# Kernel tuning notes

Hardware: AMD Instinct MI355X
Metric: run time of the kernel (lower is better)

Reference implementation:

```python
import jax, jax.numpy as jnp
import numpy as np
from jax import lax

H = 64  # hidden_size

def _lstm_layer(x, w_ih, w_hh, b_ih, b_hh):
    # x: (B, T, in). PyTorch gate order [i, f, g, o]; gates = x@W_ih^T + h@W_hh^T + b_ih + b_hh.
    B, T, _ = x.shape
    xw = jnp.einsum('bti,gi->btg', x, w_ih) + (b_ih + b_hh)  # (B, T, 4H), input projection hoisted out of scan

    def step(carry, xw_t):
        h, c = carry
        gates = xw_t + h @ w_hh.T                     # (B, 4H)
        i, f, g, o = jnp.split(gates, 4, axis=-1)
        i = jax.nn.sigmoid(i)
        f = jax.nn.sigmoid(f)
        g = jnp.tanh(g)
        o = jax.nn.sigmoid(o)
        c = f * c + i * g
        h = o * jnp.tanh(c)
        return (h, c), h

    h0 = jnp.zeros((B, H), dtype=x.dtype)
    c0 = jnp.zeros((B, H), dtype=x.dtype)
    (h_n, _), hs = lax.scan(step, (h0, c0), jnp.swapaxes(xw, 0, 1))  # hs: (T, B, H)
    return jnp.swapaxes(hs, 0, 1), h_n


def setup_inputs() -> dict:
    key = jax.random.key(0)
    ks = jax.random.split(key, 12)
    s = 1.0 / np.sqrt(H)  # PyTorch LSTM init scale
    return {
        'x':     jax.random.normal(ks[0], (2048, 512, 4), dtype=jnp.float32),
        'w_ih0': jax.random.uniform(ks[1], (4 * H, 4), jnp.float32, -s, s),
        'w_hh0': jax.random.uniform(ks[2], (4 * H, H), jnp.float32, -s, s),
        'b_ih0': jax.random.uniform(ks[3], (4 * H,), jnp.float32, -s, s),
        'b_hh0': jax.random.uniform(ks[4], (4 * H,), jnp.float32, -s, s),
        'w_ih1': jax.random.uniform(ks[5], (4 * H, H), jnp.float32, -s, s),
        'w_hh1': jax.random.uniform(ks[6], (4 * H, H), jnp.float32, -s, s),
        'b_ih1': jax.random.uniform(ks[7], (4 * H,), jnp.float32, -s, s),
        'b_hh1': jax.random.uniform(ks[8], (4 * H,), jnp.float32, -s, s),
        'fc_w':  jax.random.uniform(ks[9], (H, H), jnp.float32, -s, s),
        'fc_b':  jax.random.uniform(ks[10], (H,), jnp.float32, -s, s),
    }


def reference(x, w_ih0, w_hh0, b_ih0, b_hh0, w_ih1, w_hh1, b_ih1, b_hh1, fc_w, fc_b):
    # 2-layer LSTM (eval mode: inter-layer dropout inactive), take last layer's final hidden,
    # then Linear + tanh.
    h1_seq, _ = _lstm_layer(x, w_ih0, w_hh0, b_ih0, b_hh0)
    _, h_n = _lstm_layer(h1_seq, w_ih1, w_hh1, b_ih1, b_hh1)
    return jnp.tanh(h_n @ fc_w.T + fc_b)
```

## Files before the change

kernel.cpp:

```cpp
#include <hip/hip_runtime.h>


#define HID 64
#define TSTEPS 512
#define MB 8
#define BLK 512
#define HSTR 72
#define LOG2E  1.4426950408889634f
#define LOG2E2 2.8853900817779268f

typedef _Float16 f16;
typedef _Float16 half8 __attribute__((ext_vector_type(8)));
typedef _Float16 half4 __attribute__((ext_vector_type(4)));
typedef float f32x4 __attribute__((ext_vector_type(4)));

__device__ __forceinline__ float sig2(float y) {
    return __builtin_amdgcn_rcpf(1.0f + __builtin_amdgcn_exp2f(-y));
}
__device__ __forceinline__ float tanh2(float y) {
    return fmaf(2.0f, __builtin_amdgcn_rcpf(1.0f + __builtin_amdgcn_exp2f(-y)), -1.0f);
}

__global__ __launch_bounds__(BLK, 2) void lstm_mfma(
    const float* __restrict__ x,
    const float* __restrict__ w_ih0,
    const float* __restrict__ w_hh0,
    const float* __restrict__ b_ih0,
    const float* __restrict__ b_hh0,
    const float* __restrict__ w_ih1,
    const float* __restrict__ w_hh1,
    const float* __restrict__ b_ih1,
    const float* __restrict__ b_hh1,
    const float* __restrict__ fc_w,
    const float* __restrict__ fc_b,
    float* __restrict__ out)
{
    __shared__ f16 xs[TSTEPS * MB * 4];
    __shared__ f16 h0s[2][MB * HSTR];
    __shared__ f16 h1s[2][MB * HSTR];

    const int tid  = threadIdx.x;
    const int w    = tid >> 6;
    const int l    = tid & 63;
    const int quad = l >> 4;
    const int l15  = l & 15;
    const int wl   = w & 3;
    const bool isL0 = (w < 4);
    const int b0   = blockIdx.x * MB;

    for (int it = tid; it < MB * TSTEPS; it += BLK) {
        const int m = it >> 9;
        const int t = it & 511;
        const float4 v = *((const float4*)x + (size_t)(b0 + m) * TSTEPS + t);
        *(half4*)(xs + (t * MB + m) * 4) =
            (half4){ (f16)v.x, (f16)v.y, (f16)v.z, (f16)v.w };
    }
    for (int it = tid; it < MB * HSTR; it += BLK) {
        h0s[0][it] = (f16)0.f; h0s[1][it] = (f16)0.f;
        h1s[0][it] = (f16)0.f; h1s[1][it] = (f16)0.f;
    }

    half8 Bf[4][4];
    float biasr[4];
    const half8 Z = { (f16)0.f,(f16)0.f,(f16)0.f,(f16)0.f,
                      (f16)0.f,(f16)0.f,(f16)0.f,(f16)0.f };
    #pragma unroll
    for (int ti = 0; ti < 4; ++ti) {
        const int n = (wl + 4 * ti) * 16 + l15;
        const float sc = (ti == 2) ? LOG2E2 : LOG2E;
        if (isL0) {
            biasr[ti] = (b_ih0[n] + b_hh0[n]) * sc;
            half8 pz = Z;
            if (quad == 0) {
                const float4 v = *(const float4*)(w_ih0 + n * 4);
                pz[0] = (f16)(v.x * sc); pz[1] = (f16)(v.y * sc);
                pz[2] = (f16)(v.z * sc); pz[3] = (f16)(v.w * sc);
            }
            Bf[ti][0] = pz;
            #pragma unroll
            for (int ks = 0; ks < 2; ++ks) {
                const int ko = ks * 32 + quad * 8;
                const float4 a = *(const float4*)(w_hh0 + n * HID + ko);
                const float4 b = *(const float4*)(w_hh0 + n * HID + ko + 4);
                Bf[ti][1 + ks] = (half8){
                    (f16)(a.x*sc),(f16)(a.y*sc),(f16)(a.z*sc),(f16)(a.w*sc),
                    (f16)(b.x*sc),(f16)(b.y*sc),(f16)(b.z*sc),(f16)(b.w*sc) };
            }
            Bf[ti][3] = Z;
        } else {
            biasr[ti] = (b_ih1[n] + b_hh1[n]) * sc;
            #pragma unroll
            for (int ks = 0; ks < 2; ++ks) {
                const int ko = ks * 32 + quad * 8;
                const float4 a = *(const float4*)(w_ih1 + n * HID + ko);
                const float4 b = *(const float4*)(w_ih1 + n * HID + ko + 4);
                Bf[ti][ks] = (half8){
                    (f16)(a.x*sc),(f16)(a.y*sc),(f16)(a.z*sc),(f16)(a.w*sc),
                    (f16)(b.x*sc),(f16)(b.y*sc),(f16)(b.z*sc),(f16)(b.w*sc) };
                const float4 c = *(const float4*)(w_hh1 + n * HID + ko);
                const float4 d = *(const float4*)(w_hh1 + n * HID + ko + 4);
                Bf[ti][2 + ks] = (half8){
                    (f16)(c.x*sc),(f16)(c.y*sc),(f16)(c.z*sc),(f16)(c.w*sc),
                    (f16)(d.x*sc),(f16)(d.y*sc),(f16)(d.z*sc),(f16)(d.w*sc) };
            }
        }
    }

    const bool lo   = (quad < 2);
    const int  mrow = (quad & 1) * 4 + (lo ? 0 : 2);
    const int  uu   = wl * 16 + l15;
    const int  hb   = (l15 & 7) * HSTR + quad * 8;
    float cst0 = 0.f, cst1 = 0.f;
    __syncthreads();

    #pragma unroll 1
    for (int r = 0; r <= TSTEPS; ++r) {
        const int pr = r & 1;
        const int pv = pr ^ 1;

        if (isL0) {
            if (r < TSTEPS) {
                const half4 xv = *(const half4*)(xs + (r * MB + (l15 & 7)) * 4);
                half8 ax = Z;
                if (quad == 0) { ax[0]=xv[0]; ax[1]=xv[1]; ax[2]=xv[2]; ax[3]=xv[3]; }
                const half8 A1 = *(const half8*)(h0s[pv] + hb);
                const half8 A2 = *(const half8*)(h0s[pv] + hb + 32);
                f32x4 g[4];
                #pragma unroll
                for (int ti = 0; ti < 4; ++ti) {
                    f32x4 acc = { biasr[ti], biasr[ti], biasr[ti], biasr[ti] };
                    acc   = __builtin_amdgcn_mfma_f32_16x16x32_f16(ax, Bf[ti][0], acc, 0, 0, 0);
                    acc   = __builtin_amdgcn_mfma_f32_16x16x32_f16(A1, Bf[ti][1], acc, 0, 0, 0);
                    g[ti] = __builtin_amdgcn_mfma_f32_16x16x32_f16(A2, Bf[ti][2], acc, 0, 0, 0);
                }
                #pragma unroll
                for (int j = 0; j < 2; ++j) {
                    const float pi = lo ? g[0][j] : g[0][2 + j];
                    const float pf = lo ? g[1][j] : g[1][2 + j];
                    const float pg = lo ? g[2][j] : g[2][2 + j];
                    const float po = lo ? g[3][j] : g[3][2 + j];
                    float& c = j ? cst1 : cst0;
                    c = sig2(pf) * c + sig2(pi) * tanh2(pg);
                    h0s[pr][(mrow + j) * HSTR + uu] =
                        (f16)(sig2(po) * tanh2(c * LOG2E2));
                }
            }
        } else {
            const half8 A1 = *(const half8*)(h0s[pv] + hb);
            const half8 A2 = *(const half8*)(h0s[pv] + hb + 32);
            const half8 A3 = *(const half8*)(h1s[pr] + hb);
            const half8 A4 = *(const half8*)(h1s[pr] + hb + 32);
            f32x4 g[4];
            #pragma unroll
            for (int ti = 0; ti < 4; ++ti) {
                f32x4 acc = { biasr[ti], biasr[ti], biasr[ti], biasr[ti] };
                acc   = __builtin_amdgcn_mfma_f32_16x16x32_f16(A1, Bf[ti][0], acc, 0, 0, 0);
                acc   = __builtin_amdgcn_mfma_f32_16x16x32_f16(A2, Bf[ti][1], acc, 0, 0, 0);
                acc   = __builtin_amdgcn_mfma_f32_16x16x32_f16(A3, Bf[ti][2], acc, 0, 0, 0);
                g[ti] = __builtin_amdgcn_mfma_f32_16x16x32_f16(A4, Bf[ti][3], acc, 0, 0, 0);
            }
            const float keep = (r > 0) ? 1.f : 0.f;
            #pragma unroll
            for (int j = 0; j < 2; ++j) {
                const float pi = lo ? g[0][j] : g[0][2 + j];
                const float pf = lo ? g[1][j] : g[1][2 + j];
                const float pg = lo ? g[2][j] : g[2][2 + j];
                const float po = lo ? g[3][j] : g[3][2 + j];
                float& c = j ? cst1 : cst0;
                c = keep * (sig2(pf) * c + sig2(pi) * tanh2(pg));
                h1s[pv][(mrow + j) * HSTR + uu] =
                    (f16)(keep * sig2(po) * tanh2(c * LOG2E2));
            }
        }
        __syncthreads();
    }

    {
        const int v = tid & 63;
        const int m = tid >> 6;
        float a = fc_b[v];
        const f16* hp = h1s[1] + m * HSTR;
        const float4* wp = (const float4*)(fc_w + v * HID);
        #pragma unroll
        for (int kk = 0; kk < HID / 4; ++kk) {
            const float4 wv = wp[kk];
            a += (float)hp[kk * 4 + 0] * wv.x + (float)hp[kk * 4 + 1] * wv.y
               + (float)hp[kk * 4 + 2] * wv.z + (float)hp[kk * 4 + 3] * wv.w;
        }
        out[(size_t)(b0 + m) * HID + v] = tanh2(a * LOG2E2);
    }
}

extern "C" void kernel_launch(void* const* d_in, const int* in_sizes, int n_in,
                              void* d_out, int out_size, void* d_ws, size_t ws_size,
                              hipStream_t stream) {
    const float* x     = (const float*)d_in[0];
    const float* w_ih0 = (const float*)d_in[1];
    const float* w_hh0 = (const float*)d_in[2];
    const float* b_ih0 = (const float*)d_in[3];
    const float* b_hh0 = (const float*)d_in[4];
    const float* w_ih1 = (const float*)d_in[5];
    const float* w_hh1 = (const float*)d_in[6];
    const float* b_ih1 = (const float*)d_in[7];
    const float* b_hh1 = (const float*)d_in[8];
    const float* fc_w  = (const float*)d_in[9];
    const float* fc_b  = (const float*)d_in[10];
    float* out = (float*)d_out;

    const int B = in_sizes[0] / (TSTEPS * 4);
    lstm_mfma<<<dim3(B / MB), dim3(BLK), 0, stream>>>(
        x, w_ih0, w_hh0, b_ih0, b_hh0, w_ih1, w_hh1, b_ih1, b_hh1, fc_w, fc_b, out);
}
```

Baseline: 381.7 us.

## Split LSTM step into alternating MFMA and activation phases across layers

Restructures the time loop so that each step is split into an MFMA phase and an activation/store phase. Layer-0 warps do their MFMAs while layer-1 warps run activations, and the reverse in the next phase. This is meant to balance matrix-core and VALU/transcendental work across the two warp groups. The layer-1 hidden state becomes single-buffered. The cost is twice as many block barriers per timestep, plus a manually unrolled prologue and epilogue.

```diff
diff --git a/kernel.cpp b/kernel.cpp
--- a/kernel.cpp
+++ b/kernel.cpp
@@ -37,7 +37,7 @@
 {
     __shared__ f16 xs[TSTEPS * MB * 4];
     __shared__ f16 h0s[2][MB * HSTR];
-    __shared__ f16 h1s[2][MB * HSTR];
+    __shared__ f16 h1s[MB * HSTR];
 
     const int tid  = threadIdx.x;
     const int w    = tid >> 6;
@@ -56,8 +56,7 @@
             (half4){ (f16)v.x, (f16)v.y, (f16)v.z, (f16)v.w };
     }
     for (int it = tid; it < MB * HSTR; it += BLK) {
-        h0s[0][it] = (f16)0.f; h0s[1][it] = (f16)0.f;
-        h1s[0][it] = (f16)0.f; h1s[1][it] = (f16)0.f;
+        h0s[0][it] = (f16)0.f; h0s[1][it] = (f16)0.f; h1s[it] = (f16)0.f;
     }
 
     half8 Bf[4][4];
@@ -111,75 +110,89 @@
     const int  uu   = wl * 16 + l15;
     const int  hb   = (l15 & 7) * HSTR + quad * 8;
     float cst0 = 0.f, cst1 = 0.f;
+    f32x4 g[4];
+
+    auto l0_mfma = [&](int r, const f16* h0rd) {
+        const half4 xv = *(const half4*)(xs + (r * MB + (l15 & 7)) * 4);
+        half8 ax = Z;
+        if (quad == 0) { ax[0]=xv[0]; ax[1]=xv[1]; ax[2]=xv[2]; ax[3]=xv[3]; }
+        const half8 A1 = *(const half8*)(h0rd + hb);
+        const half8 A2 = *(const half8*)(h0rd + hb + 32);
+        #pragma unroll
+        for (int ti = 0; ti < 4; ++ti) {
+            f32x4 acc = { biasr[ti], biasr[ti], biasr[ti], biasr[ti] };
+            acc   = __builtin_amdgcn_mfma_f32_16x16x32_f16(ax, Bf[ti][0], acc, 0, 0, 0);
+            acc   = __builtin_amdgcn_mfma_f32_16x16x32_f16(A1, Bf[ti][1], acc, 0, 0, 0);
+            g[ti] = __builtin_amdgcn_mfma_f32_16x16x32_f16(A2, Bf[ti][2], acc, 0, 0, 0);
+        }
+    };
+    auto l1_mfma = [&](const f16* h0rd) {
+        const half8 A1 = *(const half8*)(h0rd + hb);
+        const half8 A2 = *(const half8*)(h0rd + hb + 32);
+        const half8 A3 = *(const half8*)(h1s + hb);
+        const half8 A4 = *(const half8*)(h1s + hb + 32);
+        #pragma unroll
+        for (int ti = 0; ti < 4; ++ti) {
+            f32x4 acc = { biasr[ti], biasr[ti], biasr[ti], biasr[ti] };
+            acc   = __builtin_amdgcn_mfma_f32_16x16x32_f16(A1, Bf[ti][0], acc, 0, 0, 0);
+            acc   = __builtin_amdgcn_mfma_f32_16x16x32_f16(A2, Bf[ti][1], acc, 0, 0, 0);
+            acc   = __builtin_amdgcn_mfma_f32_16x16x32_f16(A3, Bf[ti][2], acc, 0, 0, 0);
+            g[ti] = __builtin_amdgcn_mfma_f32_16x16x32_f16(A4, Bf[ti][3], acc, 0, 0, 0);
+        }
+    };
+    auto act_store = [&](f16* dst) {
+        #pragma unroll
+        for (int j = 0; j < 2; ++j) {
+            const float pi = lo ? g[0][j] : g[0][2 + j];
+            const float pf = lo ? g[1][j] : g[1][2 + j];
+            const float pg = lo ? g[2][j] : g[2][2 + j];
+            const float po = lo ? g[3][j] : g[3][2 + j];
+            float& c = j ? cst1 : cst0;
+            c = sig2(pf) * c + sig2(pi) * tanh2(pg);
+            dst[(mrow + j) * HSTR + uu] = (f16)(sig2(po) * tanh2(c * LOG2E2));
+        }
+    };
+
+    __syncthreads();
+
+    if (isL0) l0_mfma(0, h0s[1]);
+    __syncthreads();
+    if (isL0) act_store(h0s[0]);
+    __syncthreads();
+    if (isL0) l0_mfma(1, h0s[0]);
+    __syncthreads();
+    if (isL0) act_store(h0s[1]);
+    else      l1_mfma(h0s[0]);
     __syncthreads();
 
     #pragma unroll 1
-    for (int r = 0; r <= TSTEPS; ++r) {
-        const int pr = r & 1;
-        const int pv = pr ^ 1;
-
-        if (isL0) {
-            if (r < TSTEPS) {
-                const half4 xv = *(const half4*)(xs + (r * MB + (l15 & 7)) * 4);
-                half8 ax = Z;
-                if (quad == 0) { ax[0]=xv[0]; ax[1]=xv[1]; ax[2]=xv[2]; ax[3]=xv[3]; }
-                const half8 A1 = *(const half8*)(h0s[pv] + hb);
-                const half8 A2 = *(const half8*)(h0s[pv] + hb + 32);
-                f32x4 g[4];
-                #pragma unroll
-                for (int ti = 0; ti < 4; ++ti) {
-                    f32x4 acc = { biasr[ti], biasr[ti], biasr[ti], biasr[ti] };
-                    acc   = __builtin_amdgcn_mfma_f32_16x16x32_f16(ax, Bf[ti][0], acc, 0, 0, 0);
-                    acc   = __builtin_amdgcn_mfma_f32_16x16x32_f16(A1, Bf[ti][1], acc, 0, 0, 0);
-                    g[ti] = __builtin_amdgcn_mfma_f32_16x16x32_f16(A2, Bf[ti][2], acc, 0, 0, 0);
-                }
-                #pragma unroll
-                for (int j = 0; j < 2; ++j) {
-                    const float pi = lo ? g[0][j] : g[0][2 + j];
-                    const float pf = lo ? g[1][j] : g[1][2 + j];
-                    const float pg = lo ? g[2][j] : g[2][2 + j];
-                    const float po = lo ? g[3][j] : g[3][2 + j];
-                    float& c = j ? cst1 : cst0;
-                    c = sig2(pf) * c + sig2(pi) * tanh2(pg);
-                    h0s[pr][(mrow + j) * HSTR + uu] =
-                        (f16)(sig2(po) * tanh2(c * LOG2E2));
-                }
-            }
-        } else {
-            const half8 A1 = *(const half8*)(h0s[pv] + hb);
-            const half8 A2 = *(const half8*)(h0s[pv] + hb + 32);
-            const half8 A3 = *(const half8*)(h1s[pr] + hb);
-            const half8 A4 = *(const half8*)(h1s[pr] + hb + 32);
-            f32x4 g[4];
-            #pragma unroll
-            for (int ti = 0; ti < 4; ++ti) {
-                f32x4 acc = { biasr[ti], biasr[ti], biasr[ti], biasr[ti] };
-                acc   = __builtin_amdgcn_mfma_f32_16x16x32_f16(A1, Bf[ti][0], acc, 0, 0, 0);
-                acc   = __builtin_amdgcn_mfma_f32_16x16x32_f16(A2, Bf[ti][1], acc, 0, 0, 0);
-                acc   = __builtin_amdgcn_mfma_f32_16x16x32_f16(A3, Bf[ti][2], acc, 0, 0, 0);
-                g[ti] = __builtin_amdgcn_mfma_f32_16x16x32_f16(A4, Bf[ti][3], acc, 0, 0, 0);
-            }
-            const float keep = (r > 0) ? 1.f : 0.f;
-            #pragma unroll
-            for (int j = 0; j < 2; ++j) {
-                const float pi = lo ? g[0][j] : g[0][2 + j];
-                const float pf = lo ? g[1][j] : g[1][2 + j];
-                const float pg = lo ? g[2][j] : g[2][2 + j];
-                const float po = lo ? g[3][j] : g[3][2 + j];
-                float& c = j ? cst1 : cst0;
-                c = keep * (sig2(pf) * c + sig2(pi) * tanh2(pg));
-                h1s[pv][(mrow + j) * HSTR + uu] =
-                    (f16)(keep * sig2(po) * tanh2(c * LOG2E2));
-            }
-        }
-        __syncthreads();
-    }
+    for (int r = 2; r < TSTEPS; r += 2) {
+        if (isL0) l0_mfma(r, h0s[1]);
+        else      act_store(h1s);
+        __syncthreads();
+        if (isL0) act_store(h0s[0]);
+        else      l1_mfma(h0s[1]);
+        __syncthreads();
+        if (isL0) l0_mfma(r + 1, h0s[0]);
+        else      act_store(h1s);
+        __syncthreads();
+        if (isL0) act_store(h0s[1]);
+        else      l1_mfma(h0s[0]);
+        __syncthreads();
+    }
+
+    if (!isL0) act_store(h1s);
+    __syncthreads();
+    if (!isL0) l1_mfma(h0s[1]);
+    __syncthreads();
+    if (!isL0) act_store(h1s);
+    __syncthreads();
 
     {
         const int v = tid & 63;
         const int m = tid >> 6;
         float a = fc_b[v];
-        const f16* hp = h1s[1] + m * HSTR;
+        const f16* hp = h1s + m * HSTR;
         const float4* wp = (const float4*)(fc_w + v * HID);
         #pragma unroll
         for (int kk = 0; kk < HID / 4; ++kk) {
```

New measurement: 399.5 us. 1.05x slower.
